# Kernel optimization log

Hardware: AMD Instinct MI355X
Metric: run time of the kernel (lower is better)

## Reference

```python
import jax, jax.numpy as jnp
import numpy as np

B, N, F, H, OUT = 64, 512, 128, 256, 6


def setup_inputs() -> dict:
    key = jax.random.key(0)
    ks = jax.random.split(key, 20)
    s = 0.02
    inp = {
        "x": jax.random.normal(ks[0], (B * N, F), dtype=jnp.float32),
        "edge_index": jax.random.randint(ks[1], (2, 16), 0, B * N),
        "edge_weight": jax.random.uniform(ks[2], (16,), dtype=jnp.float32),
        "batch": jnp.repeat(jnp.arange(B, dtype=jnp.int64), N),
        "sigma": jax.random.uniform(ks[3], (1,), dtype=jnp.float32),
        "Wg": s * jax.random.normal(ks[4], (F, F)), "bg": jnp.zeros((F,)),
        "Wrel0": s * jax.random.normal(ks[5], (F, H)), "Wroot0": s * jax.random.normal(ks[6], (F, H)), "brel0": jnp.zeros((H,)),
        "Wrel1": s * jax.random.normal(ks[7], (H, H)), "Wroot1": s * jax.random.normal(ks[8], (H, H)), "brel1": jnp.zeros((H,)),
        "Wrel2": s * jax.random.normal(ks[9], (H, H)), "Wroot2": s * jax.random.normal(ks[10], (H, H)), "brel2": jnp.zeros((H,)),
        "W1": s * jax.random.normal(ks[11], (H, H)), "b1": jnp.zeros((H,)),
        "Wout": s * jax.random.normal(ks[12], (H, OUT)), "bout": jnp.zeros((OUT,)),
    }
    return inp


def _forward(x, sigma, Wg, bg, Wrel0, Wroot0, brel0, Wrel1, Wroot1, brel1,
             Wrel2, Wroot2, brel2, W1, b1, Wout, bout):
    # gdmLinear
    h = x @ Wg + bg                      # [B*N, F]
    hw = h.reshape(B, N, -1)             # to_dense_batch (equal-size windows)
    # pairwise squared distances per window -> Gaussian kernel
    sq = jnp.sum(hw * hw, axis=-1)       # [B, N]
    dist = jnp.maximum(sq[:, :, None] + sq[:, None, :]
                       - 2.0 * jnp.einsum('bnf,bmf->bnm', hw, hw), 0.0)
    A = jnp.exp(-dist / (2.0 * sigma[0] ** 2))   # [B, N, N], all > 0
    A = A * (1.0 - jnp.eye(N, dtype=A.dtype))    # nonzero extraction drops self-loops

    def conv(h, Wrel, Wroot, brel):
        # GraphConv: out_i = W_rel @ sum_j A[j,i] * h_j + b_rel + W_root @ h_i
        agg = jnp.einsum('bji,bjf->bif', A, h)
        return agg @ Wrel + brel + h @ Wroot

    h = hw
    h = jax.nn.relu(conv(h, Wrel0, Wroot0, brel0))
    h = jax.nn.relu(conv(h, Wrel1, Wroot1, brel1))
    h = conv(h, Wrel2, Wroot2, brel2)
    g = jnp.mean(h, axis=1)              # global_mean_pool (equal-size graphs)
    g = jax.nn.relu(g @ W1 + b1)
    return g @ Wout + bout               # [B, OUT]


def reference(x, edge_index, edge_weight, batch, sigma, Wg, bg,
              Wrel0, Wroot0, brel0, Wrel1, Wroot1, brel1,
              Wrel2, Wroot2, brel2, W1, b1, Wout, bout):
    # edge_index / edge_weight / batch inputs are recomputed internally by GdmGNN
    return _forward(x, sigma, Wg, bg, Wrel0, Wroot0, brel0, Wrel1, Wroot1, brel1,
                    Wrel2, Wroot2, brel2, W1, b1, Wout, bout)
```

## Files before the change

### kernel.cpp

```cpp
#include <hip/hip_runtime.h>
#include <math.h>

#define Bsz 64
#define Nn 512
#define Ff 128
#define Hh 256
#define OUTD 6
#define MTOT (Bsz * Nn)

typedef __bf16 bf16x8 __attribute__((ext_vector_type(8)));
typedef float f32x4 __attribute__((ext_vector_type(4)));
typedef int int4v __attribute__((ext_vector_type(4)));
typedef unsigned short ushort4v __attribute__((ext_vector_type(4)));

__device__ __forceinline__ unsigned short f2bf(float f) {
    unsigned u = __float_as_uint(f);
    u += 0x7FFFu + ((u >> 16) & 1u);
    return (unsigned short)(u >> 16);
}
__device__ __forceinline__ float bf2f(unsigned short s) {
    return __uint_as_float(((unsigned)s) << 16);
}

#define SWZ(r) (((r) ^ ((r) >> 2)) & 3)

__device__ __forceinline__ void async_ld16(const unsigned short* g, unsigned short* l) {
    __builtin_amdgcn_global_load_lds(
        (const __attribute__((address_space(1))) void*)g,
        (__attribute__((address_space(3))) void*)l,
        16, 0, 0);
}

#define LDH 40
#define TSZ (128 * 32)

__global__ __launch_bounds__(512) void gemm_bf16(
    const unsigned short* __restrict__ A0, const unsigned short* __restrict__ B0T,
    const unsigned short* __restrict__ A1, const unsigned short* __restrict__ B1T,
    const float* __restrict__ bias,
    unsigned short* __restrict__ C, unsigned short* __restrict__ CT,
    int M, int Ntot, int K0, int K1,
    long strideA0, long strideB0, long strideC, int flags)
{
    int bx, by, bz;
    if (flags & 8) {
        int id = blockIdx.x;
        bz = id & 63;
        int t = id >> 6;
        bx = t & 3;
        by = t >> 2;
    } else { bx = blockIdx.x; by = blockIdx.y; bz = blockIdx.z; }

    A0 += (long)bz * strideA0;
    B0T += (long)bz * strideB0;
    C += (long)bz * strideC;

    __shared__ unsigned short As[2 * TSZ];
    __shared__ unsigned short Bs[2 * TSZ];

    int tid = threadIdx.x;
    int lane = tid & 63;
    int wave = tid >> 6;
    int quad = lane >> 4, l16 = lane & 15;
    int wm = (wave >> 1) * 32, wn = (wave & 1) * 64;
    int m0 = bx * 128, n0 = by * 128;

    int sr = lane >> 2;
    int sc = lane & 3;

    int T0 = K0 >> 5, T1 = K1 >> 5;
    int T = T0 + T1;

    f32x4 acc[2][4] = {};

    auto issue = [&](int g) {
        const unsigned short* Ag; const unsigned short* Bg; int Kg, kk;
        if (g < T0) { Ag = A0; Bg = B0T; Kg = K0; kk = g << 5; }
        else        { Ag = A1; Bg = B1T; Kg = K1; kk = (g - T0) << 5; }
        unsigned short* Ad = As + (g & 1) * TSZ;
        unsigned short* Bd = Bs + (g & 1) * TSZ;
        int r = wave * 16 + sr;
        int c = sc ^ SWZ(r);
        async_ld16(Ag + (long)(m0 + r) * Kg + kk + c * 8, Ad + (wave * 16) * 32);
        async_ld16(Bg + (long)(n0 + r) * Kg + kk + c * 8, Bd + (wave * 16) * 32);
    };

    issue(0);
    for (int g = 0; g < T; ++g) {
        __syncthreads();
        if (g + 1 < T) issue(g + 1);
        const unsigned short* Ab = As + (g & 1) * TSZ;
        const unsigned short* Bb = Bs + (g & 1) * TSZ;
        bf16x8 af[2], bfr[4];
        #pragma unroll
        for (int i = 0; i < 2; ++i) {
            int r = wm + i * 16 + l16;
            af[i] = *(const bf16x8*)&Ab[r * 32 + (quad ^ SWZ(r)) * 8];
        }
        #pragma unroll
        for (int j = 0; j < 4; ++j) {
            int r = wn + j * 16 + l16;
            bfr[j] = *(const bf16x8*)&Bb[r * 32 + (quad ^ SWZ(r)) * 8];
        }
        #pragma unroll
        for (int i = 0; i < 2; ++i)
            #pragma unroll
            for (int j = 0; j < 4; ++j)
                acc[i][j] = __builtin_amdgcn_mfma_f32_16x16x32_bf16(
                    af[i], bfr[j], acc[i][j], 0, 0, 0);
    }

    int ldc = Ntot;
    #pragma unroll
    for (int i = 0; i < 2; ++i) {
        int mb = m0 + wm + i * 16 + quad * 4;
        #pragma unroll
        for (int j = 0; j < 4; ++j) {
            int n = n0 + wn + j * 16 + l16;
            f32x4 v = acc[i][j];
            float bv = bias ? bias[n] : 0.0f;
            float o0 = v[0] + bv, o1 = v[1] + bv, o2 = v[2] + bv, o3 = v[3] + bv;
            if (flags & 1) {
                o0 = fmaxf(o0, 0.f); o1 = fmaxf(o1, 0.f);
                o2 = fmaxf(o2, 0.f); o3 = fmaxf(o3, 0.f);
            }
            unsigned short s0 = f2bf(o0), s1 = f2bf(o1), s2 = f2bf(o2), s3 = f2bf(o3);
            C[(long)(mb + 0) * ldc + n] = s0;
            C[(long)(mb + 1) * ldc + n] = s1;
            C[(long)(mb + 2) * ldc + n] = s2;
            C[(long)(mb + 3) * ldc + n] = s3;
            if (CT) {
                ushort4v p; p[0] = s0; p[1] = s1; p[2] = s2; p[3] = s3;
                long ti = ((long)(mb >> 9) * Ntot + n) * 512 + (mb & 511);
                *(ushort4v*)&CT[ti] = p;
            }
        }
    }
}

__global__ __launch_bounds__(256) void h0_mfma(
    const float* __restrict__ x, const unsigned short* __restrict__ WgT,
    const float* __restrict__ bg,
    unsigned short* __restrict__ h0b, unsigned short* __restrict__ h0T,
    float* __restrict__ sqv)
{
    __shared__ unsigned short As[128 * LDH];
    __shared__ unsigned short Bs[128 * LDH];
    __shared__ float rsq[128];

    int tid = threadIdx.x;
    int lane = tid & 63;
    int wave = tid >> 6;
    int quad = lane >> 4, l16 = lane & 15;
    int wm = (wave >> 1) * 64, wn = (wave & 1) * 64;
    int m0 = blockIdx.x * 128;

    f32x4 acc[4][4] = {};

    for (int k0 = 0; k0 < Ff; k0 += 32) {
        __syncthreads();
        #pragma unroll
        for (int l = 0; l < 2; ++l) {
            int idx = tid + l * 256;
            int r = idx >> 2, ch = idx & 3;
            const float* px = x + (long)(m0 + r) * Ff + k0 + ch * 8;
            float4 xa = *(const float4*)px;
            float4 xb = *(const float4*)(px + 4);
            ushort4v pa, pb;
            pa[0] = f2bf(xa.x); pa[1] = f2bf(xa.y); pa[2] = f2bf(xa.z); pa[3] = f2bf(xa.w);
            pb[0] = f2bf(xb.x); pb[1] = f2bf(xb.y); pb[2] = f2bf(xb.z); pb[3] = f2bf(xb.w);
            *(ushort4v*)&As[r * LDH + ch * 8] = pa;
            *(ushort4v*)&As[r * LDH + ch * 8 + 4] = pb;
            int4v vb = *(const int4v*)(WgT + (long)r * Ff + k0 + ch * 8);
            *(int4v*)&Bs[r * LDH + ch * 8] = vb;
        }
        __syncthreads();
        bf16x8 af[4], bfr[4];
        #pragma unroll
        for (int i = 0; i < 4; ++i)
            af[i] = *(const bf16x8*)&As[(wm + i * 16 + l16) * LDH + quad * 8];
        #pragma unroll
        for (int j = 0; j < 4; ++j)
            bfr[j] = *(const bf16x8*)&Bs[(wn + j * 16 + l16) * LDH + quad * 8];
        #pragma unroll
        for (int i = 0; i < 4; ++i)
            #pragma unroll
            for (int j = 0; j < 4; ++j)
                acc[i][j] = __builtin_amdgcn_mfma_f32_16x16x32_bf16(
                    af[i], bfr[j], acc[i][j], 0, 0, 0);
    }

    if (tid < 128) rsq[tid] = 0.f;
    __syncthreads();

    #pragma unroll
    for (int i = 0; i < 4; ++i) {
        int lrow = wm + i * 16 + quad * 4;
        int mb = m0 + lrow;
        float rp0 = 0.f, rp1 = 0.f, rp2 = 0.f, rp3 = 0.f;
        #pragma unroll
        for (int j = 0; j < 4; ++j) {
            int n = wn + j * 16 + l16;
            f32x4 v = acc[i][j];
            float bv = bg[n];
            unsigned short s0 = f2bf(v[0] + bv), s1 = f2bf(v[1] + bv);
            unsigned short s2 = f2bf(v[2] + bv), s3 = f2bf(v[3] + bv);
            h0b[(long)(mb + 0) * Ff + n] = s0;
            h0b[(long)(mb + 1) * Ff + n] = s1;
            h0b[(long)(mb + 2) * Ff + n] = s2;
            h0b[(long)(mb + 3) * Ff + n] = s3;
            ushort4v p; p[0] = s0; p[1] = s1; p[2] = s2; p[3] = s3;
            long ti = ((long)(mb >> 9) * Ff + n) * 512 + (mb & 511);
            *(ushort4v*)&h0T[ti] = p;
            float f0 = bf2f(s0), f1 = bf2f(s1), f2 = bf2f(s2), f3 = bf2f(s3);
            rp0 += f0 * f0; rp1 += f1 * f1; rp2 += f2 * f2; rp3 += f3 * f3;
        }
        #pragma unroll
        for (int m = 1; m < 16; m <<= 1) {
            rp0 += __shfl_xor(rp0, m);
            rp1 += __shfl_xor(rp1, m);
            rp2 += __shfl_xor(rp2, m);
            rp3 += __shfl_xor(rp3, m);
        }
        if (l16 == 0) {
            atomicAdd(&rsq[lrow + 0], rp0);
            atomicAdd(&rsq[lrow + 1], rp1);
            atomicAdd(&rsq[lrow + 2], rp2);
            atomicAdd(&rsq[lrow + 3], rp3);
        }
    }
    __syncthreads();
    if (tid < 128) sqv[m0 + tid] = rsq[tid];
}

__global__ __launch_bounds__(512) void gram_A_mfma(
    const unsigned short* __restrict__ h0b, const float* __restrict__ sqv,
    const float* __restrict__ sigma, unsigned short* __restrict__ Aout,
    float* __restrict__ w)
{
    int id = blockIdx.x;
    int b = id & 63;
    int t = id >> 6;
    int i0 = (t & 3) * 128, j0 = (t >> 2) * 128;

    const unsigned short* H = h0b + (long)b * Nn * Ff;
    const float* SQ = sqv + (long)b * Nn;
    unsigned short* Ab = Aout + (long)b * Nn * Nn;

    __shared__ unsigned short Is[2 * TSZ];
    __shared__ unsigned short Js[2 * TSZ];
    __shared__ float rsum[128];

    int tid = threadIdx.x;
    int lane = tid & 63;
    int wave = tid >> 6;
    int quad = lane >> 4, l16 = lane & 15;
    int wm = (wave >> 1) * 32, wn = (wave & 1) * 64;

    int sr = lane >> 2, sc = lane & 3;

    f32x4 acc[2][4] = {};

    auto issue = [&](int g) {
        int kk = g << 5;
        unsigned short* Id = Is + (g & 1) * TSZ;
        unsigned short* Jd = Js + (g & 1) * TSZ;
        int r = wave * 16 + sr;
        int c = sc ^ SWZ(r);
        async_ld16(H + (long)(i0 + r) * Ff + kk + c * 8, Id + (wave * 16) * 32);
        async_ld16(H + (long)(j0 + r) * Ff + kk + c * 8, Jd + (wave * 16) * 32);
    };

    issue(0);
    for (int g = 0; g < (Ff >> 5); ++g) {
        __syncthreads();
        if (g + 1 < (Ff >> 5)) issue(g + 1);
        const unsigned short* Ib = Is + (g & 1) * TSZ;
        const unsigned short* Jb = Js + (g & 1) * TSZ;
        bf16x8 af[2], bfr[4];
        #pragma unroll
        for (int i = 0; i < 2; ++i) {
            int r = wm + i * 16 + l16;
            af[i] = *(const bf16x8*)&Ib[r * 32 + (quad ^ SWZ(r)) * 8];
        }
        #pragma unroll
        for (int j = 0; j < 4; ++j) {
            int r = wn + j * 16 + l16;
            bfr[j] = *(const bf16x8*)&Jb[r * 32 + (quad ^ SWZ(r)) * 8];
        }
        #pragma unroll
        for (int i = 0; i < 2; ++i)
            #pragma unroll
            for (int j = 0; j < 4; ++j)
                acc[i][j] = __builtin_amdgcn_mfma_f32_16x16x32_bf16(
                    af[i], bfr[j], acc[i][j], 0, 0, 0);
    }

    if (tid < 128) rsum[tid] = 0.f;
    __syncthreads();

    float s = sigma[0];
    float inv2s2 = 1.0f / (2.0f * s * s);
    #pragma unroll
    for (int i = 0; i < 2; ++i) {
        int lrow = wm + i * 16 + quad * 4;
        int rb = i0 + lrow;
        float rs0 = 0.f, rs1 = 0.f, rs2 = 0.f, rs3 = 0.f;
        #pragma unroll
        for (int j = 0; j < 4; ++j) {
            int c = j0 + wn + j * 16 + l16;
            float sqc = SQ[c];
            f32x4 v = acc[i][j];
            float av[4];
            #pragma unroll
            for (int r4 = 0; r4 < 4; ++r4) {
                int r = rb + r4;
                float d = fmaxf(SQ[r] + sqc - 2.0f * v[r4], 0.0f);
                unsigned short a = (r == c) ? (unsigned short)0
                                            : f2bf(__expf(-d * inv2s2));
                Ab[(long)r * Nn + c] = a;
                av[r4] = bf2f(a);
            }
            rs0 += av[0]; rs1 += av[1]; rs2 += av[2]; rs3 += av[3];
        }
        #pragma unroll
        for (int m = 1; m < 16; m <<= 1) {
            rs0 += __shfl_xor(rs0, m);
            rs1 += __shfl_xor(rs1, m);
            rs2 += __shfl_xor(rs2, m);
            rs3 += __shfl_xor(rs3, m);
        }
        if (l16 == 0) {
            atomicAdd(&rsum[lrow + 0], rs0);
            atomicAdd(&rsum[lrow + 1], rs1);
            atomicAdd(&rsum[lrow + 2], rs2);
            atomicAdd(&rsum[lrow + 3], rs3);
        }
    }
    __syncthreads();
    if (tid < 128) atomicAdd(&w[(long)b * Nn + i0 + tid], rsum[tid]);
}

__global__ __launch_bounds__(256) void convert_weights(
    const float* __restrict__ Wrel0, const float* __restrict__ Wroot0,
    const float* __restrict__ Wrel1, const float* __restrict__ Wroot1,
    const float* __restrict__ Wg,
    unsigned short* __restrict__ T0, unsigned short* __restrict__ T1,
    unsigned short* __restrict__ T2, unsigned short* __restrict__ T3,
    unsigned short* __restrict__ TG,
    float* __restrict__ w, float* __restrict__ vm)
{
    int idx = blockIdx.x * 256 + threadIdx.x;
    if (idx >= 245760) { vm[idx - 245760] = 0.f; return; }
    if (idx >= 212992) { w[idx - 212992] = 0.f; return; }
    if (idx >= 196608) {
        int e = idx - 196608;
        int o = e >> 7, i = e & 127;
        TG[e] = f2bf(Wg[(long)i * 128 + o]);
        return;
    }
    const float* src; unsigned short* dst; int kin; int e;
    if      (idx <  32768) { src = Wrel0;  dst = T0; kin = 128; e = idx; }
    else if (idx <  65536) { src = Wroot0; dst = T1; kin = 128; e = idx - 32768; }
    else if (idx < 131072) { src = Wrel1;  dst = T2; kin = 256; e = idx - 65536; }
    else                   { src = Wroot1; dst = T3; kin = 256; e = idx - 131072; }
    int o = (kin == 128) ? (e >> 7) : (e >> 8);
    int i = e & (kin - 1);
    dst[e] = f2bf(src[(long)i * 256 + o]);
}

__global__ __launch_bounds__(256) void reduce_h2(
    const unsigned short* __restrict__ h2b, const float* __restrict__ w,
    float* __restrict__ v, float* __restrict__ m)
{
    int b = blockIdx.x;
    int jc = blockIdx.y;
    int c = threadIdx.x;
    const unsigned short* H = h2b + ((long)b * Nn + jc * 64) * Hh + c;
    const float* wp = w + (long)b * Nn + jc * 64;
    float vp = 0.f, mp = 0.f;
    #pragma unroll 4
    for (int j = 0; j < 64; ++j) {
        float val = bf2f(H[(long)j * Hh]);
        mp += val;
        vp += wp[j] * val;
    }
    atomicAdd(&v[b * Hh + c], vp);
    atomicAdd(&m[b * Hh + c], mp);
}

__global__ __launch_bounds__(256) void head_kernel(
    const float* __restrict__ v, const float* __restrict__ m,
    const float* __restrict__ Wrel2, const float* __restrict__ Wroot2,
    const float* __restrict__ brel2,
    const float* __restrict__ W1, const float* __restrict__ b1,
    const float* __restrict__ Wout, const float* __restrict__ bout,
    float* __restrict__ out)
{
    int b = blockIdx.x;
    int j = threadIdx.x;
    __shared__ float vs[Hh], ms[Hh], gs[Hh], g2[Hh];
    vs[j] = v[b * Hh + j] * (1.0f / (float)Nn);
    ms[j] = m[b * Hh + j] * (1.0f / (float)Nn);
    __syncthreads();
    float s = brel2[j];
    for (int c = 0; c < Hh; ++c)
        s += vs[c] * Wrel2[c * Hh + j] + ms[c] * Wroot2[c * Hh + j];
    gs[j] = s;
    __syncthreads();
    float t = b1[j];
    for (int k = 0; k < Hh; ++k) t += gs[k] * W1[k * Hh + j];
    g2[j] = fmaxf(t, 0.f);
    __syncthreads();
    if (j < OUTD) {
        float s2 = bout[j];
        for (int k = 0; k < Hh; ++k) s2 += g2[k] * Wout[k * OUTD + j];
        out[b * OUTD + j] = s2;
    }
}

extern "C" void kernel_launch(void* const* d_in, const int* in_sizes, int n_in,
                              void* d_out, int out_size, void* d_ws, size_t ws_size,
                              hipStream_t stream) {
    const float* x      = (const float*)d_in[0];
    const float* sigma  = (const float*)d_in[4];
    const float* Wg     = (const float*)d_in[5];
    const float* bg     = (const float*)d_in[6];
    const float* Wrel0  = (const float*)d_in[7];
    const float* Wroot0 = (const float*)d_in[8];
    const float* brel0  = (const float*)d_in[9];
    const float* Wrel1  = (const float*)d_in[10];
    const float* Wroot1 = (const float*)d_in[11];
    const float* brel1  = (const float*)d_in[12];
    const float* Wrel2  = (const float*)d_in[13];
    const float* Wroot2 = (const float*)d_in[14];
    const float* brel2  = (const float*)d_in[15];
    const float* W1     = (const float*)d_in[16];
    const float* b1     = (const float*)d_in[17];
    const float* Wout   = (const float*)d_in[18];
    const float* bout   = (const float*)d_in[19];
    float* out = (float*)d_out;

    char* ws = (char*)d_ws;
    unsigned short* WgT  = (unsigned short*)(ws + 0);
    unsigned short* h0b  = (unsigned short*)(ws + 16777216);
    unsigned short* h0T  = (unsigned short*)(ws + 25165824);
    float*          sq   = (float*)(ws + 33554432);
    unsigned short* Aadj = (unsigned short*)(ws + 33685504);
    unsigned short* agg  = (unsigned short*)(ws + 67239936);
    unsigned short* h1b  = (unsigned short*)(ws + 84017152);
    unsigned short* h1T  = (unsigned short*)(ws + 100794368);
    unsigned short* h2b  = (unsigned short*)(ws + 117571584);
    unsigned short* WrelT0  = (unsigned short*)(ws + 167903232);
    unsigned short* WrootT0 = (unsigned short*)(ws + 167968768);
    unsigned short* WrelT1  = (unsigned short*)(ws + 168034304);
    unsigned short* WrootT1 = (unsigned short*)(ws + 168165376);
    float*          w    = (float*)(ws + 168558592);
    float*          v    = (float*)(ws + 168689664);
    float*          m    = (float*)(ws + 168755200);

    convert_weights<<<1088, 256, 0, stream>>>(Wrel0, Wroot0, Wrel1, Wroot1, Wg,
                                              WrelT0, WrootT0, WrelT1, WrootT1, WgT,
                                              w, v );

    h0_mfma<<<dim3(MTOT / 128, 1, 1), 256, 0, stream>>>(x, WgT, bg, h0b, h0T, sq);

    gram_A_mfma<<<dim3(16 * Bsz, 1, 1), 512, 0, stream>>>(h0b, sq, sigma, Aadj, w);

    gemm_bf16<<<dim3(4 * Bsz, 1, 1), 512, 0, stream>>>(
        Aadj, h0T, nullptr, nullptr, nullptr, agg, nullptr,
        Nn, Ff, Nn, 0,
        (long)Nn * Nn, (long)Ff * Nn, (long)Nn * Ff, 8);
    gemm_bf16<<<dim3(MTOT / 128, Hh / 128, 1), 512, 0, stream>>>(
        agg, WrelT0, h0b, WrootT0, brel0, h1b, h1T,
        MTOT, Hh, Ff, Ff, 0, 0, 0, 1);

    gemm_bf16<<<dim3(8 * Bsz, 1, 1), 512, 0, stream>>>(
        Aadj, h1T, nullptr, nullptr, nullptr, agg, nullptr,
        Nn, Hh, Nn, 0,
        (long)Nn * Nn, (long)Hh * Nn, (long)Nn * Hh, 8);
    gemm_bf16<<<dim3(MTOT / 128, Hh / 128, 1), 512, 0, stream>>>(
        agg, WrelT1, h1b, WrootT1, brel1, h2b, nullptr,
        MTOT, Hh, Hh, Hh, 0, 0, 0, 1);

    reduce_h2<<<dim3(Bsz, 8), 256, 0, stream>>>(h2b, w, v, m);

    head_kernel<<<Bsz, 256, 0, stream>>>(v, m, Wrel2, Wroot2, brel2,
                                         W1, b1, Wout, bout, out);
}
```

Baseline: 231.7 us.

## Fuse weight conversion into h0 GEMM and pooling into head; transpose A stores

Merges the weight-conversion kernel into the h0 GEMM launch as extra blocks, with the h0 blocks reading and converting Wg directly, so they no longer depend on the converted copy. Merges reduce_h2 and head_kernel into one 512-thread kernel per graph, which drops the v/m atomics and one launch. It also changes the gram kernel to write A transposed as packed 4-element stores. Fewer launches and vector stores are the intended gains. The risks are that only 64 blocks now do the pooling, and the zeroing of w in the fused kernel may race with gram_A's atomics on w.

```diff
diff --git a/kernel.cpp b/kernel.cpp
--- a/kernel.cpp
+++ b/kernel.cpp
@@ -138,12 +138,38 @@
     }
 }
 
-__global__ __launch_bounds__(256) void h0_mfma(
-    const float* __restrict__ x, const unsigned short* __restrict__ WgT,
+__global__ __launch_bounds__(256) void prep_h0(
+    const float* __restrict__ x, const float* __restrict__ Wg,
     const float* __restrict__ bg,
+    const float* __restrict__ Wrel0, const float* __restrict__ Wroot0,
+    const float* __restrict__ Wrel1, const float* __restrict__ Wroot1,
+    unsigned short* __restrict__ T0, unsigned short* __restrict__ T1,
+    unsigned short* __restrict__ T2, unsigned short* __restrict__ T3,
+    unsigned short* __restrict__ WgT,
+    float* __restrict__ w,
     unsigned short* __restrict__ h0b, unsigned short* __restrict__ h0T,
     float* __restrict__ sqv)
 {
+    if (blockIdx.x < 960) {
+        int idx = blockIdx.x * 256 + threadIdx.x;
+        if (idx >= 212992) { w[idx - 212992] = 0.f; return; }
+        if (idx >= 196608) {
+            int e = idx - 196608;
+            int o = e >> 7, i = e & 127;
+            WgT[e] = f2bf(Wg[(long)i * 128 + o]);
+            return;
+        }
+        const float* src; unsigned short* dst; int kin; int e;
+        if      (idx <  32768) { src = Wrel0;  dst = T0; kin = 128; e = idx; }
+        else if (idx <  65536) { src = Wroot0; dst = T1; kin = 128; e = idx - 32768; }
+        else if (idx < 131072) { src = Wrel1;  dst = T2; kin = 256; e = idx - 65536; }
+        else                   { src = Wroot1; dst = T3; kin = 256; e = idx - 131072; }
+        int o = (kin == 128) ? (e >> 7) : (e >> 8);
+        int i = e & (kin - 1);
+        dst[e] = f2bf(src[(long)i * 256 + o]);
+        return;
+    }
+
     __shared__ unsigned short As[128 * LDH];
     __shared__ unsigned short Bs[128 * LDH];
     __shared__ float rsq[128];
@@ -153,7 +179,7 @@
     int wave = tid >> 6;
     int quad = lane >> 4, l16 = lane & 15;
     int wm = (wave >> 1) * 64, wn = (wave & 1) * 64;
-    int m0 = blockIdx.x * 128;
+    int m0 = (blockIdx.x - 960) * 128;
 
     f32x4 acc[4][4] = {};
 
@@ -171,8 +197,14 @@
             pb[0] = f2bf(xb.x); pb[1] = f2bf(xb.y); pb[2] = f2bf(xb.z); pb[3] = f2bf(xb.w);
             *(ushort4v*)&As[r * LDH + ch * 8] = pa;
             *(ushort4v*)&As[r * LDH + ch * 8 + 4] = pb;
-            int4v vb = *(const int4v*)(WgT + (long)r * Ff + k0 + ch * 8);
-            *(int4v*)&Bs[r * LDH + ch * 8] = vb;
+            int kk = k0 + ch * 8;
+            ushort4v qa, qb;
+            #pragma unroll
+            for (int u = 0; u < 4; ++u) qa[u] = f2bf(Wg[(long)(kk + u) * 128 + r]);
+            #pragma unroll
+            for (int u = 0; u < 4; ++u) qb[u] = f2bf(Wg[(long)(kk + 4 + u) * 128 + r]);
+            *(ushort4v*)&Bs[r * LDH + ch * 8] = qa;
+            *(ushort4v*)&Bs[r * LDH + ch * 8 + 4] = qb;
         }
         __syncthreads();
         bf16x8 af[4], bfr[4];
@@ -311,6 +343,7 @@
             int c = j0 + wn + j * 16 + l16;
             float sqc = SQ[c];
             f32x4 v = acc[i][j];
+            ushort4v pk;
             float av[4];
             #pragma unroll
             for (int r4 = 0; r4 < 4; ++r4) {
@@ -318,9 +351,10 @@
                 float d = fmaxf(SQ[r] + sqc - 2.0f * v[r4], 0.0f);
                 unsigned short a = (r == c) ? (unsigned short)0
                                             : f2bf(__expf(-d * inv2s2));
-                Ab[(long)r * Nn + c] = a;
+                pk[r4] = a;
                 av[r4] = bf2f(a);
             }
+            *(ushort4v*)&Ab[(long)c * Nn + rb] = pk;
             rs0 += av[0]; rs1 += av[1]; rs2 += av[2]; rs3 += av[3];
         }
         #pragma unroll
@@ -341,56 +375,8 @@
     if (tid < 128) atomicAdd(&w[(long)b * Nn + i0 + tid], rsum[tid]);
 }
 
-__global__ __launch_bounds__(256) void convert_weights(
-    const float* __restrict__ Wrel0, const float* __restrict__ Wroot0,
-    const float* __restrict__ Wrel1, const float* __restrict__ Wroot1,
-    const float* __restrict__ Wg,
-    unsigned short* __restrict__ T0, unsigned short* __restrict__ T1,
-    unsigned short* __restrict__ T2, unsigned short* __restrict__ T3,
-    unsigned short* __restrict__ TG,
-    float* __restrict__ w, float* __restrict__ vm)
-{
-    int idx = blockIdx.x * 256 + threadIdx.x;
-    if (idx >= 245760) { vm[idx - 245760] = 0.f; return; }
-    if (idx >= 212992) { w[idx - 212992] = 0.f; return; }
-    if (idx >= 196608) {
-        int e = idx - 196608;
-        int o = e >> 7, i = e & 127;
-        TG[e] = f2bf(Wg[(long)i * 128 + o]);
-        return;
-    }
-    const float* src; unsigned short* dst; int kin; int e;
-    if      (idx <  32768) { src = Wrel0;  dst = T0; kin = 128; e = idx; }
-    else if (idx <  65536) { src = Wroot0; dst = T1; kin = 128; e = idx - 32768; }
-    else if (idx < 131072) { src = Wrel1;  dst = T2; kin = 256; e = idx - 65536; }
-    else                   { src = Wroot1; dst = T3; kin = 256; e = idx - 131072; }
-    int o = (kin == 128) ? (e >> 7) : (e >> 8);
-    int i = e & (kin - 1);
-    dst[e] = f2bf(src[(long)i * 256 + o]);
-}
-
-__global__ __launch_bounds__(256) void reduce_h2(
+__global__ __launch_bounds__(512) void pool_head(
     const unsigned short* __restrict__ h2b, const float* __restrict__ w,
-    float* __restrict__ v, float* __restrict__ m)
-{
-    int b = blockIdx.x;
-    int jc = blockIdx.y;
-    int c = threadIdx.x;
-    const unsigned short* H = h2b + ((long)b * Nn + jc * 64) * Hh + c;
-    const float* wp = w + (long)b * Nn + jc * 64;
-    float vp = 0.f, mp = 0.f;
-    #pragma unroll 4
-    for (int j = 0; j < 64; ++j) {
-        float val = bf2f(H[(long)j * Hh]);
-        mp += val;
-        vp += wp[j] * val;
-    }
-    atomicAdd(&v[b * Hh + c], vp);
-    atomicAdd(&m[b * Hh + c], mp);
-}
-
-__global__ __launch_bounds__(256) void head_kernel(
-    const float* __restrict__ v, const float* __restrict__ m,
     const float* __restrict__ Wrel2, const float* __restrict__ Wroot2,
     const float* __restrict__ brel2,
     const float* __restrict__ W1, const float* __restrict__ b1,
@@ -398,21 +384,54 @@
     float* __restrict__ out)
 {
     int b = blockIdx.x;
-    int j = threadIdx.x;
-    __shared__ float vs[Hh], ms[Hh], gs[Hh], g2[Hh];
-    vs[j] = v[b * Hh + j] * (1.0f / (float)Nn);
-    ms[j] = m[b * Hh + j] * (1.0f / (float)Nn);
-    __syncthreads();
-    float s = brel2[j];
-    for (int c = 0; c < Hh; ++c)
-        s += vs[c] * Wrel2[c * Hh + j] + ms[c] * Wroot2[c * Hh + j];
-    gs[j] = s;
-    __syncthreads();
-    float t = b1[j];
-    for (int k = 0; k < Hh; ++k) t += gs[k] * W1[k * Hh + j];
-    g2[j] = fmaxf(t, 0.f);
-    __syncthreads();
-    if (j < OUTD) {
+    int tid = threadIdx.x;
+    int c = tid & 255;
+    int half = tid >> 8;
+
+    __shared__ float vs[2][Hh], ms[2][Hh];
+    __shared__ float gs[Hh], g2[Hh];
+
+    const unsigned short* H = h2b + ((long)b * Nn + half * 256) * Hh + c;
+    const float* wp = w + (long)b * Nn + half * 256;
+    float vp = 0.f, mp = 0.f;
+    #pragma unroll 4
+    for (int j = 0; j < 256; ++j) {
+        float val = bf2f(H[(long)j * Hh]);
+        mp += val;
+        vp += wp[j] * val;
+    }
+    vs[half][c] = vp;
+    ms[half][c] = mp;
+    __syncthreads();
+
+    if (tid < Hh) {
+        int j = tid;
+        float vj, mj;
+        vj = (vs[0][j] + vs[1][j]) * (1.0f / (float)Nn);
+        mj = (ms[0][j] + ms[1][j]) * (1.0f / (float)Nn);
+        gs[j] = vj;  g2[j] = mj;
+    }
+    __syncthreads();
+    float g_j = 0.f;
+    if (tid < Hh) {
+        int j = tid;
+        float s = brel2[j];
+        for (int cc = 0; cc < Hh; ++cc)
+            s += gs[cc] * Wrel2[cc * Hh + j] + g2[cc] * Wroot2[cc * Hh + j];
+        g_j = s;
+    }
+    __syncthreads();
+    if (tid < Hh) gs[tid] = g_j;
+    __syncthreads();
+    if (tid < Hh) {
+        int j = tid;
+        float t = b1[j];
+        for (int k = 0; k < Hh; ++k) t += gs[k] * W1[k * Hh + j];
+        g2[j] = fmaxf(t, 0.f);
+    }
+    __syncthreads();
+    if (tid < OUTD) {
+        int j = tid;
         float s2 = bout[j];
         for (int k = 0; k < Hh; ++k) s2 += g2[k] * Wout[k * OUTD + j];
         out[b * OUTD + j] = s2;
@@ -456,14 +475,10 @@
     unsigned short* WrelT1  = (unsigned short*)(ws + 168034304);
     unsigned short* WrootT1 = (unsigned short*)(ws + 168165376);
     float*          w    = (float*)(ws + 168558592);
-    float*          v    = (float*)(ws + 168689664);
-    float*          m    = (float*)(ws + 168755200);
-
-    convert_weights<<<1088, 256, 0, stream>>>(Wrel0, Wroot0, Wrel1, Wroot1, Wg,
-                                              WrelT0, WrootT0, WrelT1, WrootT1, WgT,
-                                              w, v );
-
-    h0_mfma<<<dim3(MTOT / 128, 1, 1), 256, 0, stream>>>(x, WgT, bg, h0b, h0T, sq);
+
+    prep_h0<<<1216, 256, 0, stream>>>(x, Wg, bg, Wrel0, Wroot0, Wrel1, Wroot1,
+                                      WrelT0, WrootT0, WrelT1, WrootT1, WgT,
+                                      w, h0b, h0T, sq);
 
     gram_A_mfma<<<dim3(16 * Bsz, 1, 1), 512, 0, stream>>>(h0b, sq, sigma, Aadj, w);
 
@@ -483,8 +498,6 @@
         agg, WrelT1, h1b, WrootT1, brel1, h2b, nullptr,
         MTOT, Hh, Hh, Hh, 0, 0, 0, 1);
 
-    reduce_h2<<<dim3(Bsz, 8), 256, 0, stream>>>(h2b, w, v, m);
-
-    head_kernel<<<Bsz, 256, 0, stream>>>(v, m, Wrel2, Wroot2, brel2,
-                                         W1, b1, Wout, bout, out);
-}
+    pool_head<<<Bsz, 512, 0, stream>>>(h2b, w, Wrel2, Wroot2, brel2,
+                                       W1, b1, Wout, bout, out);
+}
```

Result: slower. 248.3 us (+7.2%).
